# Kernel tuning notes

Measured on AMD Instinct MI355X. Metric: run time of the kernel, lower is better.

## Reference

```python
import math
import jax, jax.numpy as jnp
import numpy as np

B, S, D, H = 2, 2048, 2048, 16
HD = D // H
EPS = 1e-6


def _precompute_freqs_cis(dim, end, theta=500000.0):
    inv_freqs = 1.0 / theta ** (np.arange(0, dim, 2, dtype=np.float32) / dim)
    t = np.arange(end, dtype=np.float32)
    freqs = np.outer(t, inv_freqs).astype(np.float32)
    # [1, end, 1, dim//2, 2] matching torch stack(cos, sin, dim=4)
    return jnp.asarray(np.stack([np.cos(freqs)[None, :, None, :], np.sin(freqs)[None, :, None, :]], axis=4))


def setup_inputs() -> dict:
    key = jax.random.key(0)
    k1, k2, k3 = jax.random.split(key, 3)
    x = jax.random.normal(k1, (B, S, D), dtype=jnp.float32)
    w_qkv = jax.random.normal(k2, (3 * D, D), dtype=jnp.float32) * 0.02
    w_out = jax.random.normal(k3, (D, D), dtype=jnp.float32) * 0.02
    attn_scale = jnp.asarray(math.log2(S * S - S), dtype=jnp.float32)
    freqs_cis = _precompute_freqs_cis(HD, S)
    return {"x": x, "w_qkv": w_qkv, "w_out": w_out, "attn_scale": attn_scale, "freqs_cis": freqs_cis}


def _apply_rotary(q, k, fc):
    # q, k: [b, s, h, hd]; fc: [1, s, 1, hd//2, 2]
    b, s, h, hd = q.shape
    qk = jnp.concatenate([q, k], axis=2).reshape(b, s, 2 * h, hd // 2, 2)
    real = qk[..., 0] * fc[..., 0] - qk[..., 1] * fc[..., 1]
    imag = qk[..., 1] * fc[..., 0] + qk[..., 0] * fc[..., 1]
    rot = jnp.stack([real, imag], axis=-1).reshape(b, s, 2 * h, hd)
    return rot[:, :, :h], rot[:, :, h:]


def reference(x, w_qkv, w_out, attn_scale, freqs_cis):
    b, s, d = x.shape
    qkv = x @ w_qkv.T                      # [b, s, 3d]
    q, k, v = jnp.split(qkv, 3, axis=2)
    q = q.reshape(b, s, H, HD)
    k = k.reshape(b, s, H, HD)
    v = v.reshape(b, s, H, HD)
    q, k = _apply_rotary(q, k, freqs_cis[:, :s])
    # -> [b, h, s, hd]
    q = q.transpose(0, 2, 1, 3)
    k = k.transpose(0, 2, 1, 3)
    v = v.transpose(0, 2, 1, 3)
    # per-head L2 norm of q/k, learned scale on q
    q = q / (jnp.linalg.norm(q, axis=-1, keepdims=True) + EPS)
    k = k / (jnp.linalg.norm(k, axis=-1, keepdims=True) + EPS)
    q = q * attn_scale
    # causal SDPA with scale=1.0
    scores = jnp.einsum('bhqd,bhkd->bhqk', q, k)
    causal = jnp.tril(jnp.ones((s, s), dtype=bool))
    scores = jnp.where(causal, scores, -jnp.inf)
    attn = jax.nn.softmax(scores, axis=-1)
    out = jnp.einsum('bhqk,bhkd->bhqd', attn, v)
    out = out.transpose(0, 2, 1, 3).reshape(b, s, d)
    return out @ w_out.T
```

## Files before the change

kernel.cpp:

```cpp
#include <hip/hip_runtime.h>
#include <stdint.h>

#define B_  2
#define S_  2048
#define D_  2048
#define H_  16
#define HD_ 128
#define D3_ 6144

typedef unsigned short u16;
typedef __attribute__((ext_vector_type(8))) __bf16 bf16x8;
typedef __attribute__((ext_vector_type(4))) float f32x4;
typedef __attribute__((ext_vector_type(8))) u16  u16x8;
typedef __attribute__((ext_vector_type(4))) u16  u16x4;
typedef __attribute__((ext_vector_type(2))) u16  u16x2;

__device__ inline u16 f2bf(float f) {
  union { float f; uint32_t u; } v; v.f = f;
  uint32_t r = v.u + 0x7FFFu + ((v.u >> 16) & 1u);
  return (u16)(r >> 16);
}
__device__ inline float bf2f(u16 u) {
  union { float f; uint32_t u; } v; v.u = ((uint32_t)u) << 16;
  return v.f;
}
__device__ inline void gload_lds16(const void* g, void* l) {
  __builtin_amdgcn_global_load_lds((const __attribute__((address_space(1))) uint32_t*)g,
                                   (__attribute__((address_space(3))) uint32_t*)l, 16, 0, 0);
}

#define TILE_SYNC() do { \
    asm volatile("s_waitcnt lgkmcnt(0)" ::: "memory"); \
    asm volatile("s_waitcnt vmcnt(0)" ::: "memory"); \
    __builtin_amdgcn_s_barrier(); \
    asm volatile("" ::: "memory"); \
  } while (0)

__global__ __launch_bounds__(256) void castk(const float* __restrict__ in, u16* __restrict__ out, int n) {
  int i = blockIdx.x * 256 + threadIdx.x;
  int n8 = n >> 3;
  if (i < n8) {
    f32x4 a = ((const f32x4*)in)[2*i];
    f32x4 b = ((const f32x4*)in)[2*i + 1];
    u16x8 o;
#pragma unroll
    for (int j = 0; j < 4; ++j) o[j] = f2bf(a[j]);
#pragma unroll
    for (int j = 0; j < 4; ++j) o[4+j] = f2bf(b[j]);
    ((u16x8*)out)[i] = o;
  }
}

template<int BF16OUT>
__global__ __launch_bounds__(512, 2) void gemm8(const u16* __restrict__ A, const u16* __restrict__ Bw,
                                                void* __restrict__ Cp, int M, int N, int K) {
  __shared__ __align__(16) u16 lds_[65536];
  char* ldsb = (char*)lds_;
  const int tid = threadIdx.x;
  const int w = tid >> 6, l = tid & 63;
  const int lr = l & 15, lg = l >> 4;
  const int wr = w >> 2, wc = w & 3;
  const int nbn = (int)gridDim.x;
  const int nwg = nbn * (int)gridDim.y;
  const int bid = (int)(blockIdx.y * gridDim.x + blockIdx.x);
  const int swz = (bid & 7) * (nwg >> 3) + (bid >> 3);
  const int bm = swz / nbn, bn = swz % nbn;

  f32x4 acc[8][4] = {};

  int row4[4], col4[4];
#pragma unroll
  for (int i = 0; i < 4; ++i) {
    int off = i*8192 + tid*16;
    row4[i] = off >> 7;
    col4[i] = (off & 127) ^ ((row4[i] & 7) << 4);
  }
  const size_t rs = (size_t)K * 2;
  const char* Ab = (const char*)A + (size_t)bm * 256 * rs;
  const char* Bb = (const char*)Bw + (size_t)bn * 256 * rs;
  const int wb = w * 1024;

#define STG(T_) do { \
    char* dA_ = ldsb + ((T_)&1)*32768; \
    char* dB_ = ldsb + 65536 + ((T_)&1)*32768; \
    _Pragma("unroll") \
    for (int i_ = 0; i_ < 4; ++i_) \
      gload_lds16(Ab + (size_t)row4[i_]*rs + (size_t)(T_)*128 + col4[i_], dA_ + i_*8192 + wb); \
    _Pragma("unroll") \
    for (int i_ = 0; i_ < 4; ++i_) \
      gload_lds16(Bb + (size_t)row4[i_]*rs + (size_t)(T_)*128 + col4[i_], dB_ + i_*8192 + wb); \
  } while (0)

#define RD_A(dst, mf, ks) do { int row_ = wr*128 + (mf)*16 + lr; \
    dst = *(const bf16x8*)(La + row_*128 + (((ks)*64 + lg*16) ^ ((row_ & 7) << 4))); } while (0)
#define RD_B(dst, nf, ks) do { int row_ = wc*64 + (nf)*16 + lr; \
    dst = *(const bf16x8*)(Lb + row_*128 + (((ks)*64 + lg*16) ^ ((row_ & 7) << 4))); } while (0)

  const int NT = K >> 6;
  STG(0);
  TILE_SYNC();

  for (int T = 0; T < NT; ++T) {
    const char* La = ldsb + (T & 1)*32768;
    const char* Lb = ldsb + 65536 + (T & 1)*32768;
    if (T + 1 < NT) STG(T + 1);

    bf16x8 a0[8], a1[8], b0[4], b1[4];
#pragma unroll
    for (int mf = 0; mf < 8; ++mf) { RD_A(a0[mf], mf, 0); RD_A(a1[mf], mf, 1); }
#pragma unroll
    for (int nf = 0; nf < 4; ++nf) { RD_B(b0[nf], nf, 0); RD_B(b1[nf], nf, 1); }
#pragma unroll
    for (int mf = 0; mf < 8; ++mf)
#pragma unroll
      for (int nf = 0; nf < 4; ++nf)
        acc[mf][nf] = __builtin_amdgcn_mfma_f32_16x16x32_bf16(a0[mf], b0[nf], acc[mf][nf], 0, 0, 0);
#pragma unroll
    for (int mf = 0; mf < 8; ++mf)
#pragma unroll
      for (int nf = 0; nf < 4; ++nf)
        acc[mf][nf] = __builtin_amdgcn_mfma_f32_16x16x32_bf16(a1[mf], b1[nf], acc[mf][nf], 0, 0, 0);
    TILE_SYNC();
  }
#undef STG
#undef RD_A
#undef RD_B

#pragma unroll
  for (int mf = 0; mf < 8; ++mf)
#pragma unroll
    for (int nf = 0; nf < 4; ++nf)
#pragma unroll
      for (int j = 0; j < 4; ++j) {
        int m = bm*256 + wr*128 + mf*16 + lg*4 + j;
        int n = bn*256 + wc*64 + nf*16 + lr;
        float v = acc[mf][nf][j];
        if (BF16OUT) ((u16*)Cp)[(size_t)m * N + n] = f2bf(v);
        else         ((float*)Cp)[(size_t)m * N + n] = v;
      }
}

template<int BF16OUT>
__global__ __launch_bounds__(256, 2) void gemm_bt(const u16* __restrict__ A, const u16* __restrict__ Bw,
                                                  void* __restrict__ Cp, int M, int N, int K) {
  __shared__ __align__(16) u16 lds_[32768];
  char* ldsb = (char*)lds_;
  const int tid = threadIdx.x;
  const int w = tid >> 6, l = tid & 63;
  const int lr = l & 15, lg = l >> 4;
  const int nwg = (int)(gridDim.x * gridDim.y);
  const int bid = (int)(blockIdx.y * gridDim.x + blockIdx.x);
  const int swz = (bid & 7) * (nwg >> 3) + (bid >> 3);
  const int bm = swz / (int)gridDim.x, bn = swz % (int)gridDim.x;
  const int wr = w >> 1, wc = w & 1;

  f32x4 acc[4][4] = {};

  int row4[4], col4[4];
#pragma unroll
  for (int i = 0; i < 4; ++i) {
    int off = i*4096 + tid*16;
    row4[i] = off >> 7;
    col4[i] = (off & 127) ^ ((row4[i] & 7) << 4);
  }
  const size_t rs = (size_t)K * 2;
  const char* Ab = (const char*)A + (size_t)bm * 128 * rs;
  const char* Bb = (const char*)Bw + (size_t)bn * 128 * rs;
  const int wb = w * 1024;

#define STG(T_) do { \
    char* dA_ = ldsb + ((T_)&1)*16384; \
    char* dB_ = ldsb + 32768 + ((T_)&1)*16384; \
    _Pragma("unroll") \
    for (int i_ = 0; i_ < 4; ++i_) \
      gload_lds16(Ab + (size_t)row4[i_]*rs + (size_t)(T_)*128 + col4[i_], dA_ + i_*4096 + wb); \
    _Pragma("unroll") \
    for (int i_ = 0; i_ < 4; ++i_) \
      gload_lds16(Bb + (size_t)row4[i_]*rs + (size_t)(T_)*128 + col4[i_], dB_ + i_*4096 + wb); \
  } while (0)

  const int NT = K >> 6;
  STG(0);
  TILE_SYNC();

  for (int T = 0; T < NT; ++T) {
    const char* La = ldsb + (T & 1)*16384;
    const char* Lb = ldsb + 32768 + (T & 1)*16384;
    if (T + 1 < NT) STG(T + 1);

    bf16x8 af[4][2], bf[4][2];
#pragma unroll
    for (int mt = 0; mt < 4; ++mt) {
      int row = wr*64 + mt*16 + lr;
#pragma unroll
      for (int ks = 0; ks < 2; ++ks)
        af[mt][ks] = *(const bf16x8*)(La + row*128 + ((ks*64 + lg*16) ^ ((row & 7) << 4)));
    }
#pragma unroll
    for (int nt = 0; nt < 4; ++nt) {
      int row = wc*64 + nt*16 + lr;
#pragma unroll
      for (int ks = 0; ks < 2; ++ks)
        bf[nt][ks] = *(const bf16x8*)(Lb + row*128 + ((ks*64 + lg*16) ^ ((row & 7) << 4)));
    }
#pragma unroll
    for (int mt = 0; mt < 4; ++mt)
#pragma unroll
      for (int nt = 0; nt < 4; ++nt)
        acc[mt][nt] = __builtin_amdgcn_mfma_f32_16x16x32_bf16(af[mt][0], bf[nt][0], acc[mt][nt], 0, 0, 0);
#pragma unroll
    for (int mt = 0; mt < 4; ++mt)
#pragma unroll
      for (int nt = 0; nt < 4; ++nt)
        acc[mt][nt] = __builtin_amdgcn_mfma_f32_16x16x32_bf16(af[mt][1], bf[nt][1], acc[mt][nt], 0, 0, 0);
    TILE_SYNC();
  }
#undef STG

#pragma unroll
  for (int mt = 0; mt < 4; ++mt)
#pragma unroll
    for (int nt = 0; nt < 4; ++nt)
#pragma unroll
      for (int j = 0; j < 4; ++j) {
        int m = bm*128 + wr*64 + mt*16 + lg*4 + j;
        int n = bn*128 + wc*64 + nt*16 + lr;
        float v = acc[mt][nt][j];
        if (BF16OUT) ((u16*)Cp)[(size_t)m * N + n] = f2bf(v);
        else         ((float*)Cp)[(size_t)m * N + n] = v;
      }
}

__global__ __launch_bounds__(256) void rope_norm(const u16* __restrict__ qkv, const float* __restrict__ fc,
                                                 const float* __restrict__ scale_p,
                                                 u16* __restrict__ Qo, u16* __restrict__ Ko) {
  int gid = blockIdx.x;
  int bs = gid >> 2;
  int s = bs & (S_ - 1);
  int b = bs >> 11;
  int w = threadIdx.x >> 6, l = threadIdx.x & 63;
  int h = (gid & 3)*4 + w;
  float2 cs = ((const float2*)fc)[(size_t)s*64 + l];
  float scale = scale_p[0] * 1.4426950408889634f;
  const u16* base = qkv + (size_t)bs * D3_;
  size_t obase = ((size_t)(b*H_ + h) * S_ + s) * HD_ + 2*l;
  {
    const u16* p = base + h*HD_ + 2*l;
    float x0 = bf2f(p[0]), x1 = bf2f(p[1]);
    float r0 = x0*cs.x - x1*cs.y;
    float r1 = x1*cs.x + x0*cs.y;
    float t = r0*r0 + r1*r1;
#pragma unroll
    for (int mk = 1; mk < 64; mk <<= 1) t += __shfl_xor(t, mk, 64);
    float inv = scale / (sqrtf(t) + 1e-6f);
    u16x2 o; o[0] = f2bf(r0*inv); o[1] = f2bf(r1*inv);
    *(u16x2*)(Qo + obase) = o;
  }
  {
    const u16* p = base + D_ + h*HD_ + 2*l;
    float x0 = bf2f(p[0]), x1 = bf2f(p[1]);
    float r0 = x0*cs.x - x1*cs.y;
    float r1 = x1*cs.x + x0*cs.y;
    float t = r0*r0 + r1*r1;
#pragma unroll
    for (int mk = 1; mk < 64; mk <<= 1) t += __shfl_xor(t, mk, 64);
    float inv = 1.0f / (sqrtf(t) + 1e-6f);
    u16x2 o; o[0] = f2bf(r0*inv); o[1] = f2bf(r1*inv);
    *(u16x2*)(Ko + obase) = o;
  }
}

__global__ __launch_bounds__(256) void v_trans(const u16* __restrict__ qkv, u16* __restrict__ Vt) {
  __shared__ u16 vt[64][136];
  int blk = blockIdx.x;
  int bh = blk >> 5, st = blk & 31;
  int b = bh >> 4, h = bh & 15;
  int s0 = st * 64;
  int tid = threadIdx.x;
#pragma unroll
  for (int i = 0; i < 4; ++i) {
    int idx = tid + i*256;
    int row = idx >> 4, ch = idx & 15;
    u16x8 v = *(const u16x8*)(qkv + (size_t)(b*S_ + s0 + row) * D3_ + 2*D_ + h*HD_ + ch*8);
    *(u16x8*)(&vt[row][ch*8]) = v;
  }
  __syncthreads();
#pragma unroll
  for (int p = 0; p < 2; ++p) {
    int d = p*64 + (tid >> 2);
    int q = (tid & 3) * 16;
    u16x8 t0, t1;
#pragma unroll
    for (int i = 0; i < 8; ++i) t0[i] = vt[q + i][d];
#pragma unroll
    for (int i = 0; i < 8; ++i) t1[i] = vt[q + 8 + i][d];
    u16* dst = Vt + ((size_t)bh * HD_ + d) * S_ + s0 + q;
    *(u16x8*)dst = t0;
    *(u16x8*)(dst + 8) = t1;
  }
}

__global__ __launch_bounds__(512) void flash_attn(const u16* __restrict__ Qh, const u16* __restrict__ Kh,
                                                  const u16* __restrict__ Vt, u16* __restrict__ AO) {
  __shared__ __align__(16) u16 lK[2][64*128];
  __shared__ __align__(16) u16 lV[128*64];
  __shared__ __align__(16) u16 lP[8][16*72];
  const int i0 = (int)blockIdx.x;
  const int k5 = i0 & 255;
  const int bh = k5 >> 3;
  const int jj = k5 & 7;
  const int qt = (i0 < 256) ? (15 - jj) : jj;
  const int tid = threadIdx.x, w = tid >> 6, l = tid & 63;
  const int lr = l & 15, lg = l >> 4;
  const int b = bh >> 4, h = bh & 15;

  bf16x8 qf[4];
  {
    const u16* qp = Qh + ((size_t)bh * S_ + qt*128 + w*16 + lr) * HD_ + lg*8;
#pragma unroll
    for (int ks = 0; ks < 4; ++ks) qf[ks] = *(const bf16x8*)(qp + ks*32);
  }
  float m0 = -__builtin_inff(), ls0 = 0.f;
  f32x4 oacc[8] = {};

  int krow[2], kcol[2], vrow[2], vcol[2], dstb[2];
#pragma unroll
  for (int p = 0; p < 2; ++p) {
    int off = p*8192 + tid*16;
    krow[p] = off >> 8; kcol[p] = (off & 255) ^ ((krow[p] & 7) << 4);
    vrow[p] = off >> 7; vcol[p] = (off & 127) ^ ((vrow[p] & 7) << 4);
    dstb[p] = p*8192 + w*1024;
  }
  const char* Kb = (const char*)(Kh + (size_t)bh * S_ * HD_);
  const char* Vb = (const char*)(Vt + (size_t)bh * HD_ * S_);

#define STAGE_K(nb, kt_) do {                                                       \
    _Pragma("unroll")                                                               \
    for (int p_ = 0; p_ < 2; ++p_)                                                  \
      gload_lds16(Kb + (size_t)((kt_)*64 + krow[p_])*256 + kcol[p_],                \
                  (char*)lK[nb] + dstb[p_]);                                        \
  } while (0)
#define STAGE_V(kt_) do {                                                           \
    _Pragma("unroll")                                                               \
    for (int p_ = 0; p_ < 2; ++p_)                                                  \
      gload_lds16(Vb + (size_t)vrow[p_]*(S_*2) + (kt_)*128 + vcol[p_],              \
                  (char*)lV + dstb[p_]);                                            \
  } while (0)

  const int nt = 2*qt + 2;
  STAGE_K(0, 0);
  STAGE_V(0);
  int cur = 0;
  for (int kt = 0; kt < nt; ++kt) {
    asm volatile("s_waitcnt vmcnt(2)" ::: "memory");
    __builtin_amdgcn_s_barrier();
    asm volatile("" ::: "memory");
    const char* lKb = (const char*)lK[cur];

    f32x4 sc[4] = {};
    __builtin_amdgcn_s_setprio(1);
#pragma unroll
    for (int ks = 0; ks < 4; ++ks) {
#pragma unroll
      for (int f = 0; f < 4; ++f) {
        int row = f*16 + lr;
        bf16x8 kf = *(const bf16x8*)(lKb + row*256 + ((ks*64 + lg*16) ^ ((row & 7) << 4)));
        sc[f] = __builtin_amdgcn_mfma_f32_16x16x32_bf16(kf, qf[ks], sc[f], 0, 0, 0);
      }
    }
    __builtin_amdgcn_s_setprio(0);
    if (kt < nt-1) STAGE_K(cur ^ 1, kt + 1);

    if (kt >= nt-2) {
#pragma unroll
      for (int f = 0; f < 4; ++f)
#pragma unroll
        for (int j = 0; j < 4; ++j)
          if (kt*64 + f*16 + lg*4 + j > qt*128 + w*16 + lr) sc[f][j] = -__builtin_inff();
    }
    float pmax = sc[0][0];
#pragma unroll
    for (int f = 0; f < 4; ++f)
#pragma unroll
      for (int j = 0; j < 4; ++j) pmax = fmaxf(pmax, sc[f][j]);
    pmax = fmaxf(pmax, __shfl_xor(pmax, 16, 64));
    pmax = fmaxf(pmax, __shfl_xor(pmax, 32, 64));
    float mn = fmaxf(m0, pmax);
    float resc = exp2f(m0 - mn);
    m0 = mn;
    float rsum = 0.f;
#pragma unroll
    for (int f = 0; f < 4; ++f)
#pragma unroll
      for (int j = 0; j < 4; ++j) {
        float p = exp2f(sc[f][j] - mn);
        sc[f][j] = p;
        rsum += p;
      }
    rsum += __shfl_xor(rsum, 16, 64);
    rsum += __shfl_xor(rsum, 32, 64);
    ls0 = ls0 * resc + rsum;
    float rescj[4];
#pragma unroll
    for (int j = 0; j < 4; ++j) rescj[j] = __shfl(resc, lg*4 + j, 64);
#pragma unroll
    for (int fd = 0; fd < 8; ++fd)
#pragma unroll
      for (int j = 0; j < 4; ++j) oacc[fd][j] *= rescj[j];
#pragma unroll
    for (int f = 0; f < 4; ++f) {
      u16x4 pk;
#pragma unroll
      for (int j = 0; j < 4; ++j) pk[j] = f2bf(sc[f][j]);
      *(u16x4*)((char*)lP[w] + lr*144 + f*32 + lg*8) = pk;
    }

    if (kt < nt-1) { asm volatile("s_waitcnt vmcnt(2)" ::: "memory"); }
    else           { asm volatile("s_waitcnt vmcnt(0)" ::: "memory"); }
    __builtin_amdgcn_s_barrier();
    asm volatile("" ::: "memory");
    __builtin_amdgcn_s_setprio(1);
#pragma unroll
    for (int ks = 0; ks < 2; ++ks) {
      bf16x8 pf = *(const bf16x8*)((const char*)lP[w] + lr*144 + ks*64 + lg*16);
#pragma unroll
      for (int fd = 0; fd < 8; ++fd) {
        int row = fd*16 + lr;
        bf16x8 vf = *(const bf16x8*)((const char*)lV + row*128 + ((ks*64 + lg*16) ^ ((row & 7) << 4)));
        oacc[fd] = __builtin_amdgcn_mfma_f32_16x16x32_bf16(pf, vf, oacc[fd], 0, 0, 0);
      }
    }
    __builtin_amdgcn_s_setprio(0);
    asm volatile("" ::: "memory");
    __builtin_amdgcn_s_barrier();
    asm volatile("" ::: "memory");
    if (kt < nt-1) STAGE_V(kt + 1);
    cur ^= 1;
  }
#undef STAGE_K
#undef STAGE_V
  float invl[4];
#pragma unroll
  for (int j = 0; j < 4; ++j) {
    float lsj = __shfl(ls0, lg*4 + j, 64);
    invl[j] = 1.0f / lsj;
  }
#pragma unroll
  for (int fd = 0; fd < 8; ++fd)
#pragma unroll
    for (int j = 0; j < 4; ++j) {
      int qq = qt*128 + w*16 + lg*4 + j;
      int dd = fd*16 + lr;
      float v = oacc[fd][j] * invl[j];
      AO[((size_t)b*S_ + qq)*D_ + h*HD_ + dd] = f2bf(v);
    }
}

extern "C" void kernel_launch(void* const* d_in, const int* in_sizes, int n_in,
                              void* d_out, int out_size, void* d_ws, size_t ws_size,
                              hipStream_t stream) {
  const float* x        = (const float*)d_in[0];
  const float* w_qkv    = (const float*)d_in[1];
  const float* w_out    = (const float*)d_in[2];
  const float* attn_sc  = (const float*)d_in[3];
  const float* freqs    = (const float*)d_in[4];

  if (ws_size < 167772160u) return;

  char* ws = (char*)d_ws;
  u16* xbf  = (u16*)(ws);
  u16* wqbf = (u16*)(ws + 16777216);
  u16* wobf = (u16*)(ws + 41943040);
  u16* qkv  = (u16*)(ws + 50331648);
  u16* Qh   = (u16*)(ws + 100663296);
  u16* Kh   = (u16*)(ws + 117440512);
  u16* Vt   = (u16*)(ws + 134217728);
  u16* AO   = (u16*)(ws + 150994944);

  castk<<<4096, 256, 0, stream>>>(x,     xbf,  8388608);
  castk<<<6144, 256, 0, stream>>>(w_qkv, wqbf, 12582912);
  castk<<<2048, 256, 0, stream>>>(w_out, wobf, 4194304);

  gemm8<1><<<dim3(24, 16), 512, 0, stream>>>(xbf, wqbf, qkv, 4096, 6144, 2048);

  rope_norm<<<16384, 256, 0, stream>>>(qkv, freqs, attn_sc, Qh, Kh);
  v_trans<<<1024, 256, 0, stream>>>(qkv, Vt);

  flash_attn<<<512, 512, 0, stream>>>(Qh, Kh, Vt, AO);

  gemm_bt<0><<<dim3(16, 32), 256, 0, stream>>>(AO, wobf, (float*)d_out, 4096, 2048, 2048);
}
```

Baseline: 278.1 us.

## Split GEMM loads into staggered A/B stages and add lazy softmax rescaling

The large GEMM kernel now issues A and B tile loads separately, prefetching B two tiles ahead and A one tile ahead. Each K-step is split into two halves of the M fragments separated by a barrier, which lowers register pressure and lets global-to-LDS loads overlap with the MFMA work. The MFMA loops in both GEMMs are interleaved so the two k-slices of each accumulator issue back to back. The attention kernel skips the running-max update and the output rescale when every lane's new max exceeds the old one by at most 8 (in log2 units); this is exact in math but lets unnormalised probabilities grow up to 256x before a rescale.

```diff
diff --git a/kernel.cpp b/kernel.cpp
--- a/kernel.cpp
+++ b/kernel.cpp
@@ -35,6 +35,8 @@
     __builtin_amdgcn_s_barrier(); \
     asm volatile("" ::: "memory"); \
   } while (0)
+
+#define BARC() do { asm volatile("" ::: "memory"); __builtin_amdgcn_s_barrier(); asm volatile("" ::: "memory"); } while (0)
 
 __global__ __launch_bounds__(256) void castk(const float* __restrict__ in, u16* __restrict__ out, int n) {
   int i = blockIdx.x * 256 + threadIdx.x;
@@ -80,12 +82,14 @@
   const char* Bb = (const char*)Bw + (size_t)bn * 256 * rs;
   const int wb = w * 1024;
 
-#define STG(T_) do { \
+#define STG_A(T_) do { \
     char* dA_ = ldsb + ((T_)&1)*32768; \
-    char* dB_ = ldsb + 65536 + ((T_)&1)*32768; \
     _Pragma("unroll") \
     for (int i_ = 0; i_ < 4; ++i_) \
       gload_lds16(Ab + (size_t)row4[i_]*rs + (size_t)(T_)*128 + col4[i_], dA_ + i_*8192 + wb); \
+  } while (0)
+#define STG_B(T_) do { \
+    char* dB_ = ldsb + 65536 + ((T_)&1)*32768; \
     _Pragma("unroll") \
     for (int i_ = 0; i_ < 4; ++i_) \
       gload_lds16(Bb + (size_t)row4[i_]*rs + (size_t)(T_)*128 + col4[i_], dB_ + i_*8192 + wb); \
@@ -97,32 +101,43 @@
     dst = *(const bf16x8*)(Lb + row_*128 + (((ks)*64 + lg*16) ^ ((row_ & 7) << 4))); } while (0)
 
   const int NT = K >> 6;
-  STG(0);
-  TILE_SYNC();
+  STG_A(0); STG_B(0); STG_B(1);
 
   for (int T = 0; T < NT; ++T) {
+    if (T < NT-1) { asm volatile("s_waitcnt vmcnt(4)" ::: "memory"); }
+    else          { asm volatile("s_waitcnt vmcnt(0)" ::: "memory"); }
+    __builtin_amdgcn_s_barrier();
+    asm volatile("" ::: "memory");
     const char* La = ldsb + (T & 1)*32768;
     const char* Lb = ldsb + 65536 + (T & 1)*32768;
-    if (T + 1 < NT) STG(T + 1);
-
-    bf16x8 a0[8], a1[8], b0[4], b1[4];
-#pragma unroll
-    for (int mf = 0; mf < 8; ++mf) { RD_A(a0[mf], mf, 0); RD_A(a1[mf], mf, 1); }
+
+    bf16x8 a0[4], a1[4], b0[4], b1[4];
+#pragma unroll
+    for (int mf = 0; mf < 4; ++mf) { RD_A(a0[mf], mf, 0); RD_A(a1[mf], mf, 1); }
 #pragma unroll
     for (int nf = 0; nf < 4; ++nf) { RD_B(b0[nf], nf, 0); RD_B(b1[nf], nf, 1); }
-#pragma unroll
-    for (int mf = 0; mf < 8; ++mf)
-#pragma unroll
-      for (int nf = 0; nf < 4; ++nf)
+    if (T + 1 < NT) STG_A(T + 1);
+#pragma unroll
+    for (int mf = 0; mf < 4; ++mf)
+#pragma unroll
+      for (int nf = 0; nf < 4; ++nf) {
         acc[mf][nf] = __builtin_amdgcn_mfma_f32_16x16x32_bf16(a0[mf], b0[nf], acc[mf][nf], 0, 0, 0);
-#pragma unroll
-    for (int mf = 0; mf < 8; ++mf)
-#pragma unroll
-      for (int nf = 0; nf < 4; ++nf)
         acc[mf][nf] = __builtin_amdgcn_mfma_f32_16x16x32_bf16(a1[mf], b1[nf], acc[mf][nf], 0, 0, 0);
-    TILE_SYNC();
-  }
-#undef STG
+      }
+    BARC();
+#pragma unroll
+    for (int mf = 0; mf < 4; ++mf) { RD_A(a0[mf], mf + 4, 0); RD_A(a1[mf], mf + 4, 1); }
+    if (T + 2 < NT) STG_B(T + 2);
+#pragma unroll
+    for (int mf = 0; mf < 4; ++mf)
+#pragma unroll
+      for (int nf = 0; nf < 4; ++nf) {
+        acc[mf+4][nf] = __builtin_amdgcn_mfma_f32_16x16x32_bf16(a0[mf], b0[nf], acc[mf+4][nf], 0, 0, 0);
+        acc[mf+4][nf] = __builtin_amdgcn_mfma_f32_16x16x32_bf16(a1[mf], b1[nf], acc[mf+4][nf], 0, 0, 0);
+      }
+  }
+#undef STG_A
+#undef STG_B
 #undef RD_A
 #undef RD_B
 
@@ -206,13 +221,10 @@
 #pragma unroll
     for (int mt = 0; mt < 4; ++mt)
 #pragma unroll
-      for (int nt = 0; nt < 4; ++nt)
+      for (int nt = 0; nt < 4; ++nt) {
         acc[mt][nt] = __builtin_amdgcn_mfma_f32_16x16x32_bf16(af[mt][0], bf[nt][0], acc[mt][nt], 0, 0, 0);
-#pragma unroll
-    for (int mt = 0; mt < 4; ++mt)
-#pragma unroll
-      for (int nt = 0; nt < 4; ++nt)
         acc[mt][nt] = __builtin_amdgcn_mfma_f32_16x16x32_bf16(af[mt][1], bf[nt][1], acc[mt][nt], 0, 0, 0);
+      }
     TILE_SYNC();
   }
 #undef STG
@@ -385,9 +397,16 @@
       for (int j = 0; j < 4; ++j) pmax = fmaxf(pmax, sc[f][j]);
     pmax = fmaxf(pmax, __shfl_xor(pmax, 16, 64));
     pmax = fmaxf(pmax, __shfl_xor(pmax, 32, 64));
-    float mn = fmaxf(m0, pmax);
-    float resc = exp2f(m0 - mn);
-    m0 = mn;
+    const int norescale = __all(pmax - m0 <= 8.0f);
+    float mn;
+    float resc = 0.f;
+    if (norescale) {
+      mn = m0;
+    } else {
+      mn = fmaxf(m0, pmax);
+      resc = exp2f(m0 - mn);
+      m0 = mn;
+    }
     float rsum = 0.f;
 #pragma unroll
     for (int f = 0; f < 4; ++f)
@@ -399,14 +418,18 @@
       }
     rsum += __shfl_xor(rsum, 16, 64);
     rsum += __shfl_xor(rsum, 32, 64);
-    ls0 = ls0 * resc + rsum;
-    float rescj[4];
-#pragma unroll
-    for (int j = 0; j < 4; ++j) rescj[j] = __shfl(resc, lg*4 + j, 64);
-#pragma unroll
-    for (int fd = 0; fd < 8; ++fd)
-#pragma unroll
-      for (int j = 0; j < 4; ++j) oacc[fd][j] *= rescj[j];
+    if (norescale) {
+      ls0 = ls0 + rsum;
+    } else {
+      ls0 = ls0 * resc + rsum;
+      float rescj[4];
+#pragma unroll
+      for (int j = 0; j < 4; ++j) rescj[j] = __shfl(resc, lg*4 + j, 64);
+#pragma unroll
+      for (int fd = 0; fd < 8; ++fd)
+#pragma unroll
+        for (int j = 0; j < 4; ++j) oacc[fd][j] *= rescj[j];
+    }
 #pragma unroll
     for (int f = 0; f < 4; ++f) {
       u16x4 pk;
```

New measurement: 271.6 us. 1.02x faster.
